# Optimization experiments

Hardware: AMD Instinct MI355X
Metric: run time of the kernel (lower is better)

The kernel has to match this reference:

```python
import jax, jax.numpy as jnp
import numpy as np

D = 1024
H = 16
HD = D // H


def setup_inputs() -> dict:
    key = jax.random.key(0)
    ks = jax.random.split(key, 9)
    s = 1.0 / np.sqrt(D)
    inp = {
        "x": jax.random.normal(ks[0], (2, 2048, D), dtype=jnp.float32),
        "Wq": jax.random.uniform(ks[1], (D, D), jnp.float32, -s, s),
        "bq": jax.random.uniform(ks[2], (D,), jnp.float32, -s, s),
        "Wk": jax.random.uniform(ks[3], (D, D), jnp.float32, -s, s),
        "bk": jax.random.uniform(ks[4], (D,), jnp.float32, -s, s),
        "Wv": jax.random.uniform(ks[5], (D, D), jnp.float32, -s, s),
        "bv": jax.random.uniform(ks[6], (D,), jnp.float32, -s, s),
        "Wo": jax.random.uniform(ks[7], (D, D), jnp.float32, -s, s),
        "bo": jax.random.uniform(ks[8], (D,), jnp.float32, -s, s),
    }
    return inp


def reference(x, Wq, bq, Wk, bk, Wv, bv, Wo, bo):
    B, S, _ = x.shape
    scale = jnp.sqrt(jnp.asarray(HD, dtype=jnp.float32))
    # QKV projections, split into heads: [B, H, S, HD]
    def proj(W, b):
        y = jnp.einsum('bsd,de->bse', x, W) + b
        return y.reshape(B, S, H, HD).transpose(0, 2, 1, 3)
    Q, K, V = proj(Wq, bq), proj(Wk, bk), proj(Wv, bv)
    scores = jnp.einsum('bhqd,bhkd->bhqk', Q, K) / scale  # [B,H,S,S]
    attn = jax.nn.softmax(scores, axis=-1)
    ctx = jnp.einsum('bhqk,bhkd->bhqd', attn, V)
    ctx = ctx.transpose(0, 2, 1, 3).reshape(B, S, D)
    return jnp.einsum('bsd,de->bse', ctx, Wo) + bo
```

## Files before the change

kernel.cpp:

```cpp
#include <hip/hip_runtime.h>
#include <hip/hip_bf16.h>

typedef __attribute__((ext_vector_type(8))) _Float16 f16x8;
typedef __attribute__((ext_vector_type(4))) float f32x4;

constexpr int Sc  = 2048;
constexpr int Dc  = 1024;
constexpr int Hc  = 16;
constexpr int HDc = 64;
constexpr int Mc  = 4096;

constexpr float ECs = 0.18033688011112042f;

__device__ __forceinline__ ushort f2h(float f) {
  return __builtin_bit_cast(ushort, (_Float16)f);
}

union US8 {
  ushort u[8];
  uint   w[4];
  f16x8  v;
};

__global__ __launch_bounds__(256) void split_x_kernel(
    const float* __restrict__ X, ushort* __restrict__ H) {
  const int i    = blockIdx.x * 256 + threadIdx.x;
  const float4 v = ((const float4*)X)[i];
  ushort4 h;
  h.x = f2h(v.x);
  h.y = f2h(v.y);
  h.z = f2h(v.z);
  h.w = f2h(v.w);
  ((ushort4*)H)[i] = h;
}

struct SplitP {
  const float* W[4];
  ushort*      Th[4];
};

__global__ __launch_bounds__(256) void split_wt_kernel(SplitP p) {
  __shared__ float T[64][69];
  const int z = blockIdx.z;
  const float* W = p.W[z];
  const int t  = threadIdx.x;
  const int c  = (t & 15) * 4;
  const int r  = t >> 4;
  const int n0 = blockIdx.x * 64, k0 = blockIdx.y * 64;
#pragma unroll
  for (int pp = 0; pp < 4; ++pp) {
    const int k    = r + pp * 16;
    const float4 v = *(const float4*)(W + (size_t)(k0 + k) * 1024 + n0 + c);
    T[k][c + 0] = v.x;
    T[k][c + 1] = v.y;
    T[k][c + 2] = v.z;
    T[k][c + 3] = v.w;
  }
  __syncthreads();
#pragma unroll
  for (int pp = 0; pp < 4; ++pp) {
    const int n = r + pp * 16;
    ushort4 h;
    h.x = f2h(T[c + 0][n]);
    h.y = f2h(T[c + 1][n]);
    h.z = f2h(T[c + 2][n]);
    h.w = f2h(T[c + 3][n]);
    *(ushort4*)(p.Th[z] + (size_t)(n0 + n) * 1024 + k0 + c) = h;
  }
}

struct GemmP {
  const ushort* Bh[3];
  const float*  bias[3];
  void*         Out[3];
};

template <bool QKV>
__global__ __launch_bounds__(256) void gemm_f16(
    const ushort* __restrict__ A, GemmP p) {
  __shared__ __align__(16) ushort As[128 * 32];
  __shared__ __align__(16) ushort Bs[128 * 32];

  const int t  = threadIdx.x;
  const int z  = blockIdx.z;
  const int m0 = blockIdx.x * 128, n0 = blockIdx.y * 128;
  const ushort* Bh  = p.Bh[z];
  const float* bias = p.bias[z];

  const int lane = t & 63, wave = t >> 6;
  const int wm = (wave & 1) * 64, wn = (wave >> 1) * 64;

  f32x4 acc[4][4];
#pragma unroll
  for (int i = 0; i < 4; ++i)
#pragma unroll
    for (int j = 0; j < 4; ++j) acc[i][j] = (f32x4){0.f, 0.f, 0.f, 0.f};

  const int am = t >> 2;
  const int ac = t & 3;
  const ushort* gA  = A  + (size_t)(m0 + am) * 1024 + ac * 8;
  const ushort* gBh = Bh + (size_t)(n0 + am) * 1024 + ac * 8;
  const int sw = ((ac + (am >> 1)) & 3) * 8;
  const int l0 = am * 32 + sw, l1 = (am + 64) * 32 + sw;

  const int fr  = lane & 15;
  const int fkb = (((lane >> 4) + (fr >> 1)) & 3) * 16;

  f16x8 rA0, rA1, rH0, rH1;
  rA0 = *(const f16x8*)(gA);
  rA1 = *(const f16x8*)(gA + 64 * 1024);
  rH0 = *(const f16x8*)(gBh);
  rH1 = *(const f16x8*)(gBh + 64 * 1024);

  for (int k0 = 0; k0 < 1024; k0 += 32) {
    __syncthreads();
    *(f16x8*)&As[l0] = rA0;
    *(f16x8*)&As[l1] = rA1;
    *(f16x8*)&Bs[l0] = rH0;
    *(f16x8*)&Bs[l1] = rH1;
    __syncthreads();

    if (k0 + 32 < 1024) {
      const int kn = k0 + 32;
      rA0 = *(const f16x8*)(gA + kn);
      rA1 = *(const f16x8*)(gA + kn + 64 * 1024);
      rH0 = *(const f16x8*)(gBh + kn);
      rH1 = *(const f16x8*)(gBh + kn + 64 * 1024);
    }

    f16x8 a[4], b_h[4];
#pragma unroll
    for (int i = 0; i < 4; ++i) {
      const int ra = (wm + i * 16 + fr) * 64 + fkb;
      const int rb = (wn + i * 16 + fr) * 64 + fkb;
      a[i]   = *(const f16x8*)((const char*)As + ra);
      b_h[i] = *(const f16x8*)((const char*)Bs + rb);
    }
#pragma unroll
    for (int i = 0; i < 4; ++i)
#pragma unroll
      for (int j = 0; j < 4; ++j)
        acc[i][j] = __builtin_amdgcn_mfma_f32_16x16x32_f16(a[i], b_h[j], acc[i][j], 0, 0, 0);
  }

  const float osc = (QKV && z == 0) ? ECs : 1.0f;
  const int cr = (lane >> 4) * 4;
  const int cc = lane & 15;
#pragma unroll
  for (int j = 0; j < 4; ++j) {
    const int n    = n0 + wn + j * 16 + cc;
    const float bv = bias[n];
#pragma unroll
    for (int i = 0; i < 4; ++i) {
      const int mb = m0 + wm + i * 16 + cr;
#pragma unroll
      for (int r = 0; r < 4; ++r) {
        const int m   = mb + r;
        const float v = (acc[i][j][r] + bv) * osc;
        if (QKV) {
          const int b = m >> 11, s = m & 2047, h = n >> 6, hd = n & 63;
          ((ushort*)p.Out[z])[(((size_t)(b * Hc + h) * Sc + s) << 6) + hd] = f2h(v);
        } else {
          ((float*)p.Out[z])[(size_t)m * 1024 + n] = v;
        }
      }
    }
  }
}

__global__ __launch_bounds__(256) void attn_mfma3(
    const ushort* __restrict__ Q, const ushort* __restrict__ K,
    const ushort* __restrict__ V, ushort* __restrict__ CTX) {
  __shared__ __align__(16) ushort Ks[64 * 64];
  __shared__ __align__(16) ushort Vt[64 * 64];

  const int t    = threadIdx.x;
  const int lane = t & 63, wave = t >> 6;
  const int c16 = lane & 15, quad = lane >> 4;
  const int bh = blockIdx.x, qt = blockIdx.y;
  const int bb = bh >> 4, hh = bh & 15;

  const ushort* Qb = Q + (size_t)bh * Sc * HDc + (size_t)qt * 128 * HDc;
  const ushort* Kb = K + (size_t)bh * Sc * HDc;
  const ushort* Vb = V + (size_t)bh * Sc * HDc;

  f16x8 aq[2][2];
#pragma unroll
  for (int mt = 0; mt < 2; ++mt)
#pragma unroll
    for (int c = 0; c < 2; ++c)
      aq[mt][c] = *(const f16x8*)(Qb + (size_t)(wave * 32 + mt * 16 + c16) * 64 + c * 32 + quad * 8);

  US8 ones_u;
#pragma unroll
  for (int e = 0; e < 8; ++e) ones_u.u[e] = 0x3C00;
  const f16x8 ones = ones_u.v;
  const f32x4 kZ = (f32x4){0.f, 0.f, 0.f, 0.f};

  f32x4 ctx[2][4], lacc[2];
#pragma unroll
  for (int mt = 0; mt < 2; ++mt) {
    lacc[mt] = (f32x4){0.f, 0.f, 0.f, 0.f};
#pragma unroll
    for (int j = 0; j < 4; ++j) ctx[mt][j] = (f32x4){0.f, 0.f, 0.f, 0.f};
  }

  const int fslot = ((quad + (c16 >> 1)) & 3) * 8;

  const int krow = t >> 2, kac = t & 3;
  const int kl = krow * 64 + ((kac + (krow >> 1)) & 3) * 8;

  const int kg = t & 15, dg = t >> 4;
  const int vc   = (kg >> 3) * 32;
  const int vq   = kg & 3;
  const int vsub = ((kg >> 2) & 1) * 4;

  const ushort* gK = Kb + (size_t)krow * 64 + kac * 8;
  const ushort* gV = Vb + (size_t)(kg * 4) * 64 + dg * 4;

  f16x8 kr0, kr1;
  ushort4 vr[4];
  kr0 = *(const f16x8*)(gK);
  kr1 = *(const f16x8*)(gK + 32);
#pragma unroll
  for (int i = 0; i < 4; ++i) vr[i] = *(const ushort4*)(gV + (size_t)i * 64);

  for (int kt = 0; kt < 32; ++kt) {
    __syncthreads();
    *(f16x8*)&Ks[kl]      = kr0;
    *(f16x8*)&Ks[kl + 32] = kr1;
    {
      const uint* w0 = (const uint*)&vr[0];
      const uint* w1 = (const uint*)&vr[1];
      const uint* w2 = (const uint*)&vr[2];
      const uint* w3 = (const uint*)&vr[3];
#pragma unroll
      for (int j = 0; j < 4; ++j) {
        const int  wd  = j >> 1;
        const uint sel = (j & 1) ? 0x07060302u : 0x05040100u;
        const uint lo  = __builtin_amdgcn_perm(w1[wd], w0[wd], sel);
        const uint hi  = __builtin_amdgcn_perm(w3[wd], w2[wd], sel);
        const int row  = dg * 4 + j;
        const int slot = (vq + (row >> 1)) & 3;
        *(uint2*)&Vt[row * 64 + vc + slot * 8 + vsub] = make_uint2(lo, hi);
      }
    }
    __syncthreads();

    if (kt < 31) {
      const size_t adv = (size_t)(kt + 1) * 64 * 64;
      kr0 = *(const f16x8*)(gK + adv);
      kr1 = *(const f16x8*)(gK + adv + 32);
#pragma unroll
      for (int i = 0; i < 4; ++i) vr[i] = *(const ushort4*)(gV + adv + (size_t)i * 64);
    }

    f32x4 st[2][4];
    __builtin_amdgcn_s_setprio(1);
#pragma unroll
    for (int j = 0; j < 4; ++j) {
      const f16x8 ak0 = *(const f16x8*)&Ks[(j * 16 + c16) * 64 + fslot];
      st[0][j] = __builtin_amdgcn_mfma_f32_16x16x32_f16(ak0, aq[0][0], kZ, 0, 0, 0);
      st[1][j] = __builtin_amdgcn_mfma_f32_16x16x32_f16(ak0, aq[1][0], kZ, 0, 0, 0);
    }
#pragma unroll
    for (int j = 0; j < 4; ++j) {
      const f16x8 ak1 = *(const f16x8*)&Ks[(j * 16 + c16) * 64 + 32 + fslot];
      st[0][j] = __builtin_amdgcn_mfma_f32_16x16x32_f16(ak1, aq[0][1], st[0][j], 0, 0, 0);
      st[1][j] = __builtin_amdgcn_mfma_f32_16x16x32_f16(ak1, aq[1][1], st[1][j], 0, 0, 0);
    }
    __builtin_amdgcn_s_setprio(0);

    US8 pf[2][2];
#pragma unroll
    for (int mt = 0; mt < 2; ++mt)
#pragma unroll
      for (int c2 = 0; c2 < 2; ++c2)
#pragma unroll
        for (int w = 0; w < 4; ++w) {
          const int jj = c2 * 2 + (w >> 1);
          const int r0 = (w & 1) * 2;
          const float pe = __builtin_amdgcn_exp2f(st[mt][jj][r0]);
          const float po = __builtin_amdgcn_exp2f(st[mt][jj][r0 + 1]);
          const auto pk = __builtin_amdgcn_cvt_pkrtz(pe, po);
          pf[mt][c2].w[w] = __builtin_bit_cast(uint, pk);
        }

    __builtin_amdgcn_s_setprio(1);
#pragma unroll
    for (int c2 = 0; c2 < 2; ++c2) {
      lacc[0] = __builtin_amdgcn_mfma_f32_16x16x32_f16(pf[0][c2].v, ones, lacc[0], 0, 0, 0);
      lacc[1] = __builtin_amdgcn_mfma_f32_16x16x32_f16(pf[1][c2].v, ones, lacc[1], 0, 0, 0);
#pragma unroll
      for (int j = 0; j < 4; ++j) {
        const f16x8 bv = *(const f16x8*)&Vt[(j * 16 + c16) * 64 + c2 * 32 + fslot];
        ctx[0][j] = __builtin_amdgcn_mfma_f32_16x16x32_f16(pf[0][c2].v, bv, ctx[0][j], 0, 0, 0);
        ctx[1][j] = __builtin_amdgcn_mfma_f32_16x16x32_f16(pf[1][c2].v, bv, ctx[1][j], 0, 0, 0);
      }
    }
    __builtin_amdgcn_s_setprio(0);
  }

#pragma unroll
  for (int mt = 0; mt < 2; ++mt) {
#pragma unroll
    for (int r = 0; r < 4; ++r) {
      const float inv = 1.f / lacc[mt][r];
      const int srow  = qt * 128 + wave * 32 + mt * 16 + quad * 4 + r;
      const size_t rb = ((size_t)(bb * Sc + srow)) * 1024 + hh * 64;
#pragma unroll
      for (int j = 0; j < 4; ++j)
        CTX[rb + j * 16 + c16] = f2h(ctx[mt][j][r] * inv);
    }
  }
}

extern "C" void kernel_launch(void* const* d_in, const int* in_sizes, int n_in,
                              void* d_out, int out_size, void* d_ws, size_t ws_size,
                              hipStream_t stream) {
  (void)in_sizes; (void)n_in; (void)out_size; (void)ws_size;
  const float* x  = (const float*)d_in[0];
  const float* Wq = (const float*)d_in[1];
  const float* bq = (const float*)d_in[2];
  const float* Wk = (const float*)d_in[3];
  const float* bk = (const float*)d_in[4];
  const float* Wv = (const float*)d_in[5];
  const float* bv = (const float*)d_in[6];
  const float* Wo = (const float*)d_in[7];
  const float* bo = (const float*)d_in[8];

  const size_t MB = 1024 * 1024;
  char* w    = (char*)d_ws;
  ushort* Qw  = (ushort*)(w + 0 * MB);
  ushort* Kw  = (ushort*)(w + 8 * MB);
  ushort* Vw  = (ushort*)(w + 16 * MB);
  ushort* Cw  = (ushort*)(w + 24 * MB);
  ushort* Xh  = (ushort*)(w + 32 * MB);
  ushort* WT  = (ushort*)(w + 40 * MB);
  ushort* Whq = WT + 0 * 1048576;
  ushort* Whk = WT + 1 * 1048576;
  ushort* Whv = WT + 2 * 1048576;
  ushort* Who = WT + 3 * 1048576;

  const dim3 blk(256);

  split_x_kernel<<<4096, blk, 0, stream>>>(x, Xh);

  SplitP sp;
  sp.W[0] = Wq; sp.W[1] = Wk; sp.W[2] = Wv; sp.W[3] = Wo;
  sp.Th[0] = Whq; sp.Th[1] = Whk; sp.Th[2] = Whv; sp.Th[3] = Who;
  split_wt_kernel<<<dim3(16, 16, 4), blk, 0, stream>>>(sp);

  GemmP pq;
  pq.Bh[0] = Whq; pq.Bh[1] = Whk; pq.Bh[2] = Whv;
  pq.bias[0] = bq; pq.bias[1] = bk; pq.bias[2] = bv;
  pq.Out[0] = Qw; pq.Out[1] = Kw; pq.Out[2] = Vw;
  gemm_f16<true><<<dim3(Mc / 128, Dc / 128, 3), blk, 0, stream>>>(Xh, pq);

  attn_mfma3<<<dim3(2 * Hc, Sc / 128), blk, 0, stream>>>(Qw, Kw, Vw, Cw);

  GemmP po;
  po.Bh[0] = po.Bh[1] = po.Bh[2] = Who;
  po.bias[0] = po.bias[1] = po.bias[2] = bo;
  po.Out[0] = po.Out[1] = po.Out[2] = d_out;
  gemm_f16<false><<<dim3(Mc / 128, Dc / 128, 1), blk, 0, stream>>>(Cw, po);
}
```

Before: 199.2 us.

## Double-buffer K/V tiles in attention LDS and flatten the grid

The attention kernel now keeps two LDS buffers for K and V-transposed. Each iteration writes the next tile into the spare buffer while computing on the current one, so the loop needs one barrier per step instead of two and the global prefetch runs two tiles ahead. The grid is flattened to 1D with the batch-head index varying fastest. This changes the order in which workgroups are dispatched. The cost is twice the LDS per workgroup, which may lower occupancy, and more registers held live for the deeper prefetch.

```diff
diff --git a/kernel.cpp b/kernel.cpp
--- a/kernel.cpp
+++ b/kernel.cpp
@@ -171,13 +171,14 @@
 __global__ __launch_bounds__(256) void attn_mfma3(
     const ushort* __restrict__ Q, const ushort* __restrict__ K,
     const ushort* __restrict__ V, ushort* __restrict__ CTX) {
-  __shared__ __align__(16) ushort Ks[64 * 64];
-  __shared__ __align__(16) ushort Vt[64 * 64];
+  __shared__ __align__(16) ushort Ks[2][64 * 64];
+  __shared__ __align__(16) ushort Vt[2][64 * 64];
 
   const int t    = threadIdx.x;
   const int lane = t & 63, wave = t >> 6;
   const int c16 = lane & 15, quad = lane >> 4;
-  const int bh = blockIdx.x, qt = blockIdx.y;
+  const int wg = blockIdx.x;
+  const int bh = wg & 31, qt = wg >> 5;
   const int bb = bh >> 4, hh = bh & 15;
 
   const ushort* Qb = Q + (size_t)bh * Sc * HDc + (size_t)qt * 128 * HDc;
@@ -220,16 +221,41 @@
 
   f16x8 kr0, kr1;
   ushort4 vr[4];
+
   kr0 = *(const f16x8*)(gK);
   kr1 = *(const f16x8*)(gK + 32);
 #pragma unroll
   for (int i = 0; i < 4; ++i) vr[i] = *(const ushort4*)(gV + (size_t)i * 64);
 
+  *(f16x8*)&Ks[0][kl]      = kr0;
+  *(f16x8*)&Ks[0][kl + 32] = kr1;
+  {
+    const uint* w0 = (const uint*)&vr[0];
+    const uint* w1 = (const uint*)&vr[1];
+    const uint* w2 = (const uint*)&vr[2];
+    const uint* w3 = (const uint*)&vr[3];
+#pragma unroll
+    for (int j = 0; j < 4; ++j) {
+      const int  wd  = j >> 1;
+      const uint sel = (j & 1) ? 0x07060302u : 0x05040100u;
+      const uint lo  = __builtin_amdgcn_perm(w1[wd], w0[wd], sel);
+      const uint hi  = __builtin_amdgcn_perm(w3[wd], w2[wd], sel);
+      const int row  = dg * 4 + j;
+      const int slot = (vq + (row >> 1)) & 3;
+      *(uint2*)&Vt[0][row * 64 + vc + slot * 8 + vsub] = make_uint2(lo, hi);
+    }
+  }
+  kr0 = *(const f16x8*)(gK + 4096);
+  kr1 = *(const f16x8*)(gK + 4096 + 32);
+#pragma unroll
+  for (int i = 0; i < 4; ++i) vr[i] = *(const ushort4*)(gV + 4096 + (size_t)i * 64);
+  __syncthreads();
+
+  int p = 0;
   for (int kt = 0; kt < 32; ++kt) {
-    __syncthreads();
-    *(f16x8*)&Ks[kl]      = kr0;
-    *(f16x8*)&Ks[kl + 32] = kr1;
-    {
+    if (kt < 31) {
+      *(f16x8*)&Ks[p ^ 1][kl]      = kr0;
+      *(f16x8*)&Ks[p ^ 1][kl + 32] = kr1;
       const uint* w0 = (const uint*)&vr[0];
       const uint* w1 = (const uint*)&vr[1];
       const uint* w2 = (const uint*)&vr[2];
@@ -242,30 +268,31 @@
         const uint hi  = __builtin_amdgcn_perm(w3[wd], w2[wd], sel);
         const int row  = dg * 4 + j;
         const int slot = (vq + (row >> 1)) & 3;
-        *(uint2*)&Vt[row * 64 + vc + slot * 8 + vsub] = make_uint2(lo, hi);
+        *(uint2*)&Vt[p ^ 1][row * 64 + vc + slot * 8 + vsub] = make_uint2(lo, hi);
       }
     }
-    __syncthreads();
-
-    if (kt < 31) {
-      const size_t adv = (size_t)(kt + 1) * 64 * 64;
+    if (kt < 30) {
+      const size_t adv = (size_t)(kt + 2) * 64 * 64;
       kr0 = *(const f16x8*)(gK + adv);
       kr1 = *(const f16x8*)(gK + adv + 32);
 #pragma unroll
       for (int i = 0; i < 4; ++i) vr[i] = *(const ushort4*)(gV + adv + (size_t)i * 64);
     }
 
+    const ushort* ksb = Ks[p];
+    const ushort* vtb = Vt[p];
+
     f32x4 st[2][4];
     __builtin_amdgcn_s_setprio(1);
 #pragma unroll
     for (int j = 0; j < 4; ++j) {
-      const f16x8 ak0 = *(const f16x8*)&Ks[(j * 16 + c16) * 64 + fslot];
+      const f16x8 ak0 = *(const f16x8*)&ksb[(j * 16 + c16) * 64 + fslot];
       st[0][j] = __builtin_amdgcn_mfma_f32_16x16x32_f16(ak0, aq[0][0], kZ, 0, 0, 0);
       st[1][j] = __builtin_amdgcn_mfma_f32_16x16x32_f16(ak0, aq[1][0], kZ, 0, 0, 0);
     }
 #pragma unroll
     for (int j = 0; j < 4; ++j) {
-      const f16x8 ak1 = *(const f16x8*)&Ks[(j * 16 + c16) * 64 + 32 + fslot];
+      const f16x8 ak1 = *(const f16x8*)&ksb[(j * 16 + c16) * 64 + 32 + fslot];
       st[0][j] = __builtin_amdgcn_mfma_f32_16x16x32_f16(ak1, aq[0][1], st[0][j], 0, 0, 0);
       st[1][j] = __builtin_amdgcn_mfma_f32_16x16x32_f16(ak1, aq[1][1], st[1][j], 0, 0, 0);
     }
@@ -293,12 +320,15 @@
       lacc[1] = __builtin_amdgcn_mfma_f32_16x16x32_f16(pf[1][c2].v, ones, lacc[1], 0, 0, 0);
 #pragma unroll
       for (int j = 0; j < 4; ++j) {
-        const f16x8 bv = *(const f16x8*)&Vt[(j * 16 + c16) * 64 + c2 * 32 + fslot];
+        const f16x8 bv = *(const f16x8*)&vtb[(j * 16 + c16) * 64 + c2 * 32 + fslot];
         ctx[0][j] = __builtin_amdgcn_mfma_f32_16x16x32_f16(pf[0][c2].v, bv, ctx[0][j], 0, 0, 0);
         ctx[1][j] = __builtin_amdgcn_mfma_f32_16x16x32_f16(pf[1][c2].v, bv, ctx[1][j], 0, 0, 0);
       }
     }
     __builtin_amdgcn_s_setprio(0);
+
+    p ^= 1;
+    __syncthreads();
   }
 
 #pragma unroll
@@ -357,7 +387,7 @@
   pq.Out[0] = Qw; pq.Out[1] = Kw; pq.Out[2] = Vw;
   gemm_f16<true><<<dim3(Mc / 128, Dc / 128, 3), blk, 0, stream>>>(Xh, pq);
 
-  attn_mfma3<<<dim3(2 * Hc, Sc / 128), blk, 0, stream>>>(Qw, Kw, Vw, Cw);
+  attn_mfma3<<<dim3(512), blk, 0, stream>>>(Qw, Kw, Vw, Cw);
 
   GemmP po;
   po.Bh[0] = po.Bh[1] = po.Bh[2] = Who;
```

Result: no change. 199.3 us (+0.1%).

## Double per-block query tile in attention and merge prep conversion kernels

Applied to the files above, without the earlier changes.

The attention kernel now has each workgroup process 256 query rows instead of 128, with each wave handling two 32-row halves. Every K/V tile staged in shared memory is therefore reused across twice as many queries, which halves K/V global traffic and staging work. The trade-off is more accumulator registers, only 256 workgroups for the 256 CUs, and a launch bound of 2 blocks per CU. Separately, the x-to-fp16 conversion and the weight-transpose kernels are fused into a single launch to save one kernel launch.

```diff
diff --git a/kernel.cpp b/kernel.cpp
--- a/kernel.cpp
+++ b/kernel.cpp
@@ -22,31 +22,35 @@
   f16x8  v;
 };
 
-__global__ __launch_bounds__(256) void split_x_kernel(
-    const float* __restrict__ X, ushort* __restrict__ H) {
-  const int i    = blockIdx.x * 256 + threadIdx.x;
-  const float4 v = ((const float4*)X)[i];
-  ushort4 h;
-  h.x = f2h(v.x);
-  h.y = f2h(v.y);
-  h.z = f2h(v.z);
-  h.w = f2h(v.w);
-  ((ushort4*)H)[i] = h;
-}
-
 struct SplitP {
   const float* W[4];
   ushort*      Th[4];
 };
 
-__global__ __launch_bounds__(256) void split_wt_kernel(SplitP p) {
+__global__ __launch_bounds__(256) void prep_kernel(
+    const float* __restrict__ X, ushort* __restrict__ Xh, SplitP p) {
   __shared__ float T[64][69];
-  const int z = blockIdx.z;
+  const int wid = blockIdx.x;
+  const int t   = threadIdx.x;
+  if (wid < 4096) {
+    const int i    = wid * 256 + t;
+    const float4 v = ((const float4*)X)[i];
+    ushort4 h;
+    h.x = f2h(v.x);
+    h.y = f2h(v.y);
+    h.z = f2h(v.z);
+    h.w = f2h(v.w);
+    ((ushort4*)Xh)[i] = h;
+    return;
+  }
+  const int w2 = wid - 4096;
+  const int z  = w2 >> 8;
+  const int by = (w2 >> 4) & 15;
+  const int bx = w2 & 15;
   const float* W = p.W[z];
-  const int t  = threadIdx.x;
   const int c  = (t & 15) * 4;
   const int r  = t >> 4;
-  const int n0 = blockIdx.x * 64, k0 = blockIdx.y * 64;
+  const int n0 = bx * 64, k0 = by * 64;
 #pragma unroll
   for (int pp = 0; pp < 4; ++pp) {
     const int k    = r + pp * 16;
@@ -168,7 +172,7 @@
   }
 }
 
-__global__ __launch_bounds__(256) void attn_mfma3(
+__global__ __launch_bounds__(256, 2) void attn_mfma3(
     const ushort* __restrict__ Q, const ushort* __restrict__ K,
     const ushort* __restrict__ V, ushort* __restrict__ CTX) {
   __shared__ __align__(16) ushort Ks[64 * 64];
@@ -177,19 +181,23 @@
   const int t    = threadIdx.x;
   const int lane = t & 63, wave = t >> 6;
   const int c16 = lane & 15, quad = lane >> 4;
-  const int bh = blockIdx.x, qt = blockIdx.y;
+  const int wg = blockIdx.x;
+  const int bh = wg & 31, qt = wg >> 5;
   const int bb = bh >> 4, hh = bh & 15;
 
-  const ushort* Qb = Q + (size_t)bh * Sc * HDc + (size_t)qt * 128 * HDc;
+  const ushort* Qb = Q + (size_t)bh * Sc * HDc + (size_t)qt * 256 * HDc;
   const ushort* Kb = K + (size_t)bh * Sc * HDc;
   const ushort* Vb = V + (size_t)bh * Sc * HDc;
 
-  f16x8 aq[2][2];
-#pragma unroll
-  for (int mt = 0; mt < 2; ++mt)
-#pragma unroll
-    for (int c = 0; c < 2; ++c)
-      aq[mt][c] = *(const f16x8*)(Qb + (size_t)(wave * 32 + mt * 16 + c16) * 64 + c * 32 + quad * 8);
+  f16x8 aq[2][2][2];
+#pragma unroll
+  for (int qh = 0; qh < 2; ++qh)
+#pragma unroll
+    for (int mt = 0; mt < 2; ++mt)
+#pragma unroll
+      for (int c = 0; c < 2; ++c)
+        aq[qh][mt][c] = *(const f16x8*)(Qb +
+            (size_t)(wave * 64 + qh * 32 + mt * 16 + c16) * 64 + c * 32 + quad * 8);
 
   US8 ones_u;
 #pragma unroll
@@ -197,13 +205,15 @@
   const f16x8 ones = ones_u.v;
   const f32x4 kZ = (f32x4){0.f, 0.f, 0.f, 0.f};
 
-  f32x4 ctx[2][4], lacc[2];
-#pragma unroll
-  for (int mt = 0; mt < 2; ++mt) {
-    lacc[mt] = (f32x4){0.f, 0.f, 0.f, 0.f};
-#pragma unroll
-    for (int j = 0; j < 4; ++j) ctx[mt][j] = (f32x4){0.f, 0.f, 0.f, 0.f};
-  }
+  f32x4 ctx[2][2][4], lacc[2][2];
+#pragma unroll
+  for (int qh = 0; qh < 2; ++qh)
+#pragma unroll
+    for (int mt = 0; mt < 2; ++mt) {
+      lacc[qh][mt] = (f32x4){0.f, 0.f, 0.f, 0.f};
+#pragma unroll
+      for (int j = 0; j < 4; ++j) ctx[qh][mt][j] = (f32x4){0.f, 0.f, 0.f, 0.f};
+    }
 
   const int fslot = ((quad + (c16 >> 1)) & 3) * 8;
 
@@ -255,64 +265,69 @@
       for (int i = 0; i < 4; ++i) vr[i] = *(const ushort4*)(gV + adv + (size_t)i * 64);
     }
 
-    f32x4 st[2][4];
-    __builtin_amdgcn_s_setprio(1);
-#pragma unroll
-    for (int j = 0; j < 4; ++j) {
-      const f16x8 ak0 = *(const f16x8*)&Ks[(j * 16 + c16) * 64 + fslot];
-      st[0][j] = __builtin_amdgcn_mfma_f32_16x16x32_f16(ak0, aq[0][0], kZ, 0, 0, 0);
-      st[1][j] = __builtin_amdgcn_mfma_f32_16x16x32_f16(ak0, aq[1][0], kZ, 0, 0, 0);
-    }
-#pragma unroll
-    for (int j = 0; j < 4; ++j) {
-      const f16x8 ak1 = *(const f16x8*)&Ks[(j * 16 + c16) * 64 + 32 + fslot];
-      st[0][j] = __builtin_amdgcn_mfma_f32_16x16x32_f16(ak1, aq[0][1], st[0][j], 0, 0, 0);
-      st[1][j] = __builtin_amdgcn_mfma_f32_16x16x32_f16(ak1, aq[1][1], st[1][j], 0, 0, 0);
-    }
-    __builtin_amdgcn_s_setprio(0);
-
-    US8 pf[2][2];
-#pragma unroll
-    for (int mt = 0; mt < 2; ++mt)
-#pragma unroll
-      for (int c2 = 0; c2 < 2; ++c2)
-#pragma unroll
-        for (int w = 0; w < 4; ++w) {
-          const int jj = c2 * 2 + (w >> 1);
-          const int r0 = (w & 1) * 2;
-          const float pe = __builtin_amdgcn_exp2f(st[mt][jj][r0]);
-          const float po = __builtin_amdgcn_exp2f(st[mt][jj][r0 + 1]);
-          const auto pk = __builtin_amdgcn_cvt_pkrtz(pe, po);
-          pf[mt][c2].w[w] = __builtin_bit_cast(uint, pk);
+#pragma unroll
+    for (int qh = 0; qh < 2; ++qh) {
+      f32x4 st[2][4];
+      __builtin_amdgcn_s_setprio(1);
+#pragma unroll
+      for (int j = 0; j < 4; ++j) {
+        const f16x8 ak0 = *(const f16x8*)&Ks[(j * 16 + c16) * 64 + fslot];
+        st[0][j] = __builtin_amdgcn_mfma_f32_16x16x32_f16(ak0, aq[qh][0][0], kZ, 0, 0, 0);
+        st[1][j] = __builtin_amdgcn_mfma_f32_16x16x32_f16(ak0, aq[qh][1][0], kZ, 0, 0, 0);
+      }
+#pragma unroll
+      for (int j = 0; j < 4; ++j) {
+        const f16x8 ak1 = *(const f16x8*)&Ks[(j * 16 + c16) * 64 + 32 + fslot];
+        st[0][j] = __builtin_amdgcn_mfma_f32_16x16x32_f16(ak1, aq[qh][0][1], st[0][j], 0, 0, 0);
+        st[1][j] = __builtin_amdgcn_mfma_f32_16x16x32_f16(ak1, aq[qh][1][1], st[1][j], 0, 0, 0);
+      }
+      __builtin_amdgcn_s_setprio(0);
+
+      US8 pf[2][2];
+#pragma unroll
+      for (int mt = 0; mt < 2; ++mt)
+#pragma unroll
+        for (int c2 = 0; c2 < 2; ++c2)
+#pragma unroll
+          for (int w = 0; w < 4; ++w) {
+            const int jj = c2 * 2 + (w >> 1);
+            const int r0 = (w & 1) * 2;
+            const float pe = __builtin_amdgcn_exp2f(st[mt][jj][r0]);
+            const float po = __builtin_amdgcn_exp2f(st[mt][jj][r0 + 1]);
+            const auto pk = __builtin_amdgcn_cvt_pkrtz(pe, po);
+            pf[mt][c2].w[w] = __builtin_bit_cast(uint, pk);
+          }
+
+      __builtin_amdgcn_s_setprio(1);
+#pragma unroll
+      for (int c2 = 0; c2 < 2; ++c2) {
+        lacc[qh][0] = __builtin_amdgcn_mfma_f32_16x16x32_f16(pf[0][c2].v, ones, lacc[qh][0], 0, 0, 0);
+        lacc[qh][1] = __builtin_amdgcn_mfma_f32_16x16x32_f16(pf[1][c2].v, ones, lacc[qh][1], 0, 0, 0);
+#pragma unroll
+        for (int j = 0; j < 4; ++j) {
+          const f16x8 bv = *(const f16x8*)&Vt[(j * 16 + c16) * 64 + c2 * 32 + fslot];
+          ctx[qh][0][j] = __builtin_amdgcn_mfma_f32_16x16x32_f16(pf[0][c2].v, bv, ctx[qh][0][j], 0, 0, 0);
+          ctx[qh][1][j] = __builtin_amdgcn_mfma_f32_16x16x32_f16(pf[1][c2].v, bv, ctx[qh][1][j], 0, 0, 0);
         }
-
-    __builtin_amdgcn_s_setprio(1);
-#pragma unroll
-    for (int c2 = 0; c2 < 2; ++c2) {
-      lacc[0] = __builtin_amdgcn_mfma_f32_16x16x32_f16(pf[0][c2].v, ones, lacc[0], 0, 0, 0);
-      lacc[1] = __builtin_amdgcn_mfma_f32_16x16x32_f16(pf[1][c2].v, ones, lacc[1], 0, 0, 0);
-#pragma unroll
-      for (int j = 0; j < 4; ++j) {
-        const f16x8 bv = *(const f16x8*)&Vt[(j * 16 + c16) * 64 + c2 * 32 + fslot];
-        ctx[0][j] = __builtin_amdgcn_mfma_f32_16x16x32_f16(pf[0][c2].v, bv, ctx[0][j], 0, 0, 0);
-        ctx[1][j] = __builtin_amdgcn_mfma_f32_16x16x32_f16(pf[1][c2].v, bv, ctx[1][j], 0, 0, 0);
-      }
-    }
-    __builtin_amdgcn_s_setprio(0);
-  }
-
-#pragma unroll
-  for (int mt = 0; mt < 2; ++mt) {
-#pragma unroll
-    for (int r = 0; r < 4; ++r) {
-      const float inv = 1.f / lacc[mt][r];
-      const int srow  = qt * 128 + wave * 32 + mt * 16 + quad * 4 + r;
-      const size_t rb = ((size_t)(bb * Sc + srow)) * 1024 + hh * 64;
-#pragma unroll
-      for (int j = 0; j < 4; ++j)
-        CTX[rb + j * 16 + c16] = f2h(ctx[mt][j][r] * inv);
-    }
-  }
+      }
+      __builtin_amdgcn_s_setprio(0);
+    }
+  }
+
+#pragma unroll
+  for (int qh = 0; qh < 2; ++qh)
+#pragma unroll
+    for (int mt = 0; mt < 2; ++mt) {
+#pragma unroll
+      for (int r = 0; r < 4; ++r) {
+        const float inv = 1.f / lacc[qh][mt][r];
+        const int srow  = qt * 256 + wave * 64 + qh * 32 + mt * 16 + quad * 4 + r;
+        const size_t rb = ((size_t)(bb * Sc + srow)) * 1024 + hh * 64;
+#pragma unroll
+        for (int j = 0; j < 4; ++j)
+          CTX[rb + j * 16 + c16] = f2h(ctx[qh][mt][j][r] * inv);
+      }
+    }
 }
 
 extern "C" void kernel_launch(void* const* d_in, const int* in_sizes, int n_in,
@@ -344,12 +359,10 @@
 
   const dim3 blk(256);
 
-  split_x_kernel<<<4096, blk, 0, stream>>>(x, Xh);
-
   SplitP sp;
   sp.W[0] = Wq; sp.W[1] = Wk; sp.W[2] = Wv; sp.W[3] = Wo;
   sp.Th[0] = Whq; sp.Th[1] = Whk; sp.Th[2] = Whv; sp.Th[3] = Who;
-  split_wt_kernel<<<dim3(16, 16, 4), blk, 0, stream>>>(sp);
+  prep_kernel<<<dim3(5120), blk, 0, stream>>>(x, Xh, sp);
 
   GemmP pq;
   pq.Bh[0] = Whq; pq.Bh[1] = Whk; pq.Bh[2] = Whv;
@@ -357,7 +370,7 @@
   pq.Out[0] = Qw; pq.Out[1] = Kw; pq.Out[2] = Vw;
   gemm_f16<true><<<dim3(Mc / 128, Dc / 128, 3), blk, 0, stream>>>(Xh, pq);
 
-  attn_mfma3<<<dim3(2 * Hc, Sc / 128), blk, 0, stream>>>(Qw, Kw, Vw, Cw);
+  attn_mfma3<<<dim3(256), blk, 0, stream>>>(Qw, Kw, Vw, Cw);
 
   GemmP po;
   po.Bh[0] = po.Bh[1] = po.Bh[2] = Who;
```

Measured after the change: 196.8 us. Within noise of the previous version (-1.2%).

## Merge prep kernels and widen attention blocks to 512 threads with split K/V loaders

Applied to the files above, without the earlier changes.

Fuses the x-to-fp16 conversion and the weight transpose/convert into one prep kernel launch, removing a launch. The attention kernel now uses 512-thread blocks covering 256 query rows, so each K/V tile staged in shared memory serves twice as many queries. Half the threads load K and half load V, which halves per-thread global load work. The grid shrinks to 256 blocks with launch_bounds(512,1), which may cap occupancy and latency hiding.

```diff
diff --git a/kernel.cpp b/kernel.cpp
--- a/kernel.cpp
+++ b/kernel.cpp
@@ -22,31 +22,35 @@
   f16x8  v;
 };
 
-__global__ __launch_bounds__(256) void split_x_kernel(
-    const float* __restrict__ X, ushort* __restrict__ H) {
-  const int i    = blockIdx.x * 256 + threadIdx.x;
-  const float4 v = ((const float4*)X)[i];
-  ushort4 h;
-  h.x = f2h(v.x);
-  h.y = f2h(v.y);
-  h.z = f2h(v.z);
-  h.w = f2h(v.w);
-  ((ushort4*)H)[i] = h;
-}
-
 struct SplitP {
   const float* W[4];
   ushort*      Th[4];
 };
 
-__global__ __launch_bounds__(256) void split_wt_kernel(SplitP p) {
+__global__ __launch_bounds__(256) void prep_kernel(
+    const float* __restrict__ X, ushort* __restrict__ Xh, SplitP p) {
   __shared__ float T[64][69];
-  const int z = blockIdx.z;
+  const int wid = blockIdx.x;
+  const int t   = threadIdx.x;
+  if (wid < 4096) {
+    const int i    = wid * 256 + t;
+    const float4 v = ((const float4*)X)[i];
+    ushort4 h;
+    h.x = f2h(v.x);
+    h.y = f2h(v.y);
+    h.z = f2h(v.z);
+    h.w = f2h(v.w);
+    ((ushort4*)Xh)[i] = h;
+    return;
+  }
+  const int w2 = wid - 4096;
+  const int z  = w2 >> 8;
+  const int by = (w2 >> 4) & 15;
+  const int bx = w2 & 15;
   const float* W = p.W[z];
-  const int t  = threadIdx.x;
   const int c  = (t & 15) * 4;
   const int r  = t >> 4;
-  const int n0 = blockIdx.x * 64, k0 = blockIdx.y * 64;
+  const int n0 = bx * 64, k0 = by * 64;
 #pragma unroll
   for (int pp = 0; pp < 4; ++pp) {
     const int k    = r + pp * 16;
@@ -168,7 +172,7 @@
   }
 }
 
-__global__ __launch_bounds__(256) void attn_mfma3(
+__global__ __launch_bounds__(512, 1) void attn_mfma3(
     const ushort* __restrict__ Q, const ushort* __restrict__ K,
     const ushort* __restrict__ V, ushort* __restrict__ CTX) {
   __shared__ __align__(16) ushort Ks[64 * 64];
@@ -177,10 +181,11 @@
   const int t    = threadIdx.x;
   const int lane = t & 63, wave = t >> 6;
   const int c16 = lane & 15, quad = lane >> 4;
-  const int bh = blockIdx.x, qt = blockIdx.y;
+  const int wg = blockIdx.x;
+  const int bh = wg & 31, qt = wg >> 5;
   const int bb = bh >> 4, hh = bh & 15;
 
-  const ushort* Qb = Q + (size_t)bh * Sc * HDc + (size_t)qt * 128 * HDc;
+  const ushort* Qb = Q + (size_t)bh * Sc * HDc + (size_t)qt * 256 * HDc;
   const ushort* Kb = K + (size_t)bh * Sc * HDc;
   const ushort* Vb = V + (size_t)bh * Sc * HDc;
 
@@ -189,7 +194,8 @@
   for (int mt = 0; mt < 2; ++mt)
 #pragma unroll
     for (int c = 0; c < 2; ++c)
-      aq[mt][c] = *(const f16x8*)(Qb + (size_t)(wave * 32 + mt * 16 + c16) * 64 + c * 32 + quad * 8);
+      aq[mt][c] = *(const f16x8*)(Qb +
+          (size_t)(wave * 32 + mt * 16 + c16) * 64 + c * 32 + quad * 8);
 
   US8 ones_u;
 #pragma unroll
@@ -207,10 +213,13 @@
 
   const int fslot = ((quad + (c16 >> 1)) & 3) * 8;
 
-  const int krow = t >> 2, kac = t & 3;
+  const bool isK = (t < 256);
+  const int ts  = isK ? t : (t - 256);
+
+  const int krow = ts >> 2, kac = ts & 3;
   const int kl = krow * 64 + ((kac + (krow >> 1)) & 3) * 8;
 
-  const int kg = t & 15, dg = t >> 4;
+  const int kg = ts & 15, dg = ts >> 4;
   const int vc   = (kg >> 3) * 32;
   const int vq   = kg & 3;
   const int vsub = ((kg >> 2) & 1) * 4;
@@ -220,16 +229,20 @@
 
   f16x8 kr0, kr1;
   ushort4 vr[4];
-  kr0 = *(const f16x8*)(gK);
-  kr1 = *(const f16x8*)(gK + 32);
-#pragma unroll
-  for (int i = 0; i < 4; ++i) vr[i] = *(const ushort4*)(gV + (size_t)i * 64);
+  if (isK) {
+    kr0 = *(const f16x8*)(gK);
+    kr1 = *(const f16x8*)(gK + 32);
+  } else {
+#pragma unroll
+    for (int i = 0; i < 4; ++i) vr[i] = *(const ushort4*)(gV + (size_t)i * 64);
+  }
 
   for (int kt = 0; kt < 32; ++kt) {
     __syncthreads();
-    *(f16x8*)&Ks[kl]      = kr0;
-    *(f16x8*)&Ks[kl + 32] = kr1;
-    {
+    if (isK) {
+      *(f16x8*)&Ks[kl]      = kr0;
+      *(f16x8*)&Ks[kl + 32] = kr1;
+    } else {
       const uint* w0 = (const uint*)&vr[0];
       const uint* w1 = (const uint*)&vr[1];
       const uint* w2 = (const uint*)&vr[2];
@@ -249,10 +262,13 @@
 
     if (kt < 31) {
       const size_t adv = (size_t)(kt + 1) * 64 * 64;
-      kr0 = *(const f16x8*)(gK + adv);
-      kr1 = *(const f16x8*)(gK + adv + 32);
-#pragma unroll
-      for (int i = 0; i < 4; ++i) vr[i] = *(const ushort4*)(gV + adv + (size_t)i * 64);
+      if (isK) {
+        kr0 = *(const f16x8*)(gK + adv);
+        kr1 = *(const f16x8*)(gK + adv + 32);
+      } else {
+#pragma unroll
+        for (int i = 0; i < 4; ++i) vr[i] = *(const ushort4*)(gV + adv + (size_t)i * 64);
+      }
     }
 
     f32x4 st[2][4];
@@ -306,7 +322,7 @@
 #pragma unroll
     for (int r = 0; r < 4; ++r) {
       const float inv = 1.f / lacc[mt][r];
-      const int srow  = qt * 128 + wave * 32 + mt * 16 + quad * 4 + r;
+      const int srow  = qt * 256 + wave * 32 + mt * 16 + quad * 4 + r;
       const size_t rb = ((size_t)(bb * Sc + srow)) * 1024 + hh * 64;
 #pragma unroll
       for (int j = 0; j < 4; ++j)
@@ -344,12 +360,10 @@
 
   const dim3 blk(256);
 
-  split_x_kernel<<<4096, blk, 0, stream>>>(x, Xh);
-
   SplitP sp;
   sp.W[0] = Wq; sp.W[1] = Wk; sp.W[2] = Wv; sp.W[3] = Wo;
   sp.Th[0] = Whq; sp.Th[1] = Whk; sp.Th[2] = Whv; sp.Th[3] = Who;
-  split_wt_kernel<<<dim3(16, 16, 4), blk, 0, stream>>>(sp);
+  prep_kernel<<<dim3(5120), blk, 0, stream>>>(x, Xh, sp);
 
   GemmP pq;
   pq.Bh[0] = Whq; pq.Bh[1] = Whk; pq.Bh[2] = Whv;
@@ -357,7 +371,7 @@
   pq.Out[0] = Qw; pq.Out[1] = Kw; pq.Out[2] = Vw;
   gemm_f16<true><<<dim3(Mc / 128, Dc / 128, 3), blk, 0, stream>>>(Xh, pq);
 
-  attn_mfma3<<<dim3(2 * Hc, Sc / 128), blk, 0, stream>>>(Qw, Kw, Vw, Cw);
+  attn_mfma3<<<dim3(256), dim3(512), 0, stream>>>(Qw, Kw, Vw, Cw);
 
   GemmP po;
   po.Bh[0] = po.Bh[1] = po.Bh[2] = Who;
```

After: 204.0 us. 2.4% more time.
